# Optimization experiments

Hardware: AMD Instinct MI355X
Metric: run time of the kernel (lower is better)

Reference implementation:

```python
import jax, jax.numpy as jnp
import numpy as np
from jax import lax

BATCH = 2560
N_CLS = 128    # QP decision dim n
N_INEQ = 128   # number of inequality constraints
N_FEAT = 128
IPM_ITERS = 20
SIGMA = 0.1    # centering parameter


def setup_inputs() -> dict:
    key = jax.random.key(0)
    k1, k2, k3, k4, k5 = jax.random.split(key, 5)
    x = jax.random.normal(k1, (BATCH, N_FEAT), dtype=jnp.float32)
    # symmetric positive-definite Q (qpth requires PD Q)
    A = jax.random.normal(k2, (N_CLS, N_CLS), dtype=jnp.float32) / np.sqrt(N_CLS).astype(np.float32)
    Q = A @ A.T + 1e-4 * jnp.eye(N_CLS, dtype=jnp.float32)
    p = jax.random.normal(k3, (BATCH, N_CLS), dtype=jnp.float32)
    G = jax.random.uniform(k4, (N_INEQ, N_CLS), minval=-1.0, maxval=1.0, dtype=jnp.float32)
    # h > 0 so z = 0 is strictly feasible -> well-conditioned IPM
    h = jax.random.uniform(k5, (N_INEQ,), dtype=jnp.float32) + 1.0
    return {"x": x, "Q": Q, "p": p, "G": G, "h": h, "m": 1}


def _qp_solve(Q, p, G, h, iters=IPM_ITERS, sigma=SIGMA):
    """Batched primal-dual interior-point solve of
       min_z 1/2 z'Qz + p'z  s.t.  Gz + s = h, s >= 0.
    Q: [n,n] shared; p: [B,n]; G: [m,n] shared; h: [m] shared."""
    B, n = p.shape
    mI = G.shape[0]
    z = jnp.zeros((B, n), p.dtype)
    s = jnp.ones((B, mI), p.dtype)
    lam = jnp.ones((B, mI), p.dtype)
    GT = G.T

    def frac_to_boundary(v, dv):
        safe = jnp.where(dv < 0, dv, -1.0)
        r = jnp.where(dv < 0, -v / safe, 1e9)
        return jnp.minimum(1.0, 0.99 * jnp.min(r, axis=1, keepdims=True))

    def step(carry, _):
        z, s, lam = carry
        r_d = z @ Q.T + p + lam @ G          # [B,n]  Qz + p + G'lam
        r_p = z @ GT + s - h                 # [B,m]  Gz + s - h
        mu = jnp.mean(s * lam, axis=1, keepdims=True)
        r_c = s * lam - sigma * mu           # [B,m]
        d = lam / s                          # [B,m]
        # reduced KKT: (Q + G' D G) dz = -r_d + G'((r_c - lam*r_p)/s)
        M = Q[None] + jnp.einsum('ki,bk,kj->bij', G, d, G)  # [B,n,n]
        rhs = -r_d + ((r_c - lam * r_p) / s) @ G             # [B,n]
        dz = jnp.linalg.solve(M, rhs[..., None])[..., 0]
        ds = -r_p - dz @ GT
        dlam = (-r_c - lam * ds) / s
        a = jnp.minimum(frac_to_boundary(s, ds), frac_to_boundary(lam, dlam))
        return (z + a * dz, s + a * ds, lam + a * dlam), None

    (z, s, lam), _ = lax.scan(step, (z, s, lam), None, length=iters)
    return z


def reference(x, Q, p, G, h, m):
    # m==1 path of OptNet.forward: p stays [B,n], Q shared [n,n]
    pf = p.T if m > 1 else p
    z = _qp_solve(Q.astype(jnp.float32), pf.astype(jnp.float32),
                  G.astype(jnp.float32), h.astype(jnp.float32))
    out = z.reshape(10, -1)  # faithful to x.view(10, -1)
    return jax.nn.log_softmax(out, axis=1)
```

## Files before the change

### kernel.cpp

```cpp
#include <hip/hip_runtime.h>
#include <math.h>


#define B_TOT 2560
#define TB 32
#define NB (B_TOT/TB)

__device__ __forceinline__ int ROFF(int i){ return (i*(i+1))>>1; }
__device__ __forceinline__ int rowStart(int i){
  int a=i>>2, b=i&3;
  return ((a+1)*((a<<1)+b))<<2;
}
#define TRI_SZ 8448

__device__ __forceinline__ int rowOfIdx(int idx){
  int i = (int)((sqrtf(8.f*(float)idx+1.f)-1.f)*0.5f);
  while (((i+1)*(i+2)>>1) <= idx) ++i;
  while (((i*(i+1))>>1) > idx) --i;
  return i;
}

__device__ __forceinline__ void chol_diag_gj(float* tri, int c0, int lane){
  float rowA[16], rowW[16];
  const int r = lane;
  #pragma unroll
  for (int j=0;j<16;++j){ rowA[j]=0.f; rowW[j]=0.f; }
  if (r < 16){
    const float* src = &tri[rowStart(c0+r)+c0];
    #pragma unroll
    for (int q=0;q<4;++q){
      if (q <= (r>>2)){
        float4 w = *(const float4*)&src[4*q];
        rowA[4*q+0]=w.x; rowA[4*q+1]=w.y; rowA[4*q+2]=w.z; rowA[4*q+3]=w.w;
      }
    }
    #pragma unroll
    for (int j=0;j<16;++j) if (j>r) rowA[j]=0.f;
    #pragma unroll
    for (int j=0;j<16;++j) rowW[j] = (j==r)?1.f:0.f;
  }
  #pragma unroll
  for (int k=0;k<16;++k){
    float akk = __shfl(rowA[k], k, 64);
    akk = fmaxf(akk, 1e-12f);
    float linv = rsqrtf(akk);
    float lrk = rowA[k]*linv;
    if (r==k){
      #pragma unroll
      for (int c=0;c<16;++c) rowW[c] *= linv;
    }
    #pragma unroll
    for (int j=k+1;j<16;++j){
      float ljk = __shfl(lrk, j, 64);
      if (r>=j) rowA[j] = fmaf(-lrk, ljk, rowA[j]);
    }
    #pragma unroll
    for (int c=0;c<=k;++c){
      float wkc = __shfl(rowW[c], k, 64);
      if (r>k) rowW[c] = fmaf(-lrk, wkc, rowW[c]);
    }
  }
  if (r < 16){
    float* dst = &tri[rowStart(c0+r)+c0];
    #pragma unroll
    for (int q=0;q<4;++q){
      if (q <= (r>>2)){
        float4 w; w.x=rowW[4*q+0]; w.y=rowW[4*q+1]; w.z=rowW[4*q+2]; w.w=rowW[4*q+3];
        *(float4*)&dst[4*q] = w;
      }
    }
  }
}

__device__ void chol_factor(float* tri, int t, int lane, int wid){
  for (int kb=0; kb<8; ++kb){
    const int c0 = kb*16;
    if (wid==(kb&3)) chol_diag_gj(tri, c0, lane);
    __syncthreads();
    const int rem = 112 - c0;
    if (t < rem){
      const int r = c0+16+t;
      const int rb = rowStart(r)+c0;
      float a[16];
      #pragma unroll
      for (int q=0;q<4;++q){
        float4 w = *(const float4*)&tri[rb+4*q];
        a[4*q+0]=w.x; a[4*q+1]=w.y; a[4*q+2]=w.z; a[4*q+3]=w.w;
      }
      float x[16];
      #pragma unroll
      for (int c=0;c<16;++c){
        float acc=0.f;
        const int lb = rowStart(c0+c)+c0;
        #pragma unroll
        for (int q=0;q<=(c>>2);++q){
          float4 w = *(const float4*)&tri[lb+4*q];
          if (4*q+0<=c) acc = fmaf(w.x, a[4*q+0], acc);
          if (4*q+1<=c) acc = fmaf(w.y, a[4*q+1], acc);
          if (4*q+2<=c) acc = fmaf(w.z, a[4*q+2], acc);
          if (4*q+3<=c) acc = fmaf(w.w, a[4*q+3], acc);
        }
        x[c]=acc;
      }
      #pragma unroll
      for (int q=0;q<4;++q){
        float4 w; w.x=x[4*q+0]; w.y=x[4*q+1]; w.z=x[4*q+2]; w.w=x[4*q+3];
        *(float4*)&tri[rb+4*q] = w;
      }
    }
    __syncthreads();
    if (rem > 0){
      const int base = c0+16;
      const int R = rem>>2;
      const int ntile = (R*(R+1))>>1;
      for (int idx=t; idx<ntile; idx+=256){
        int I = rowOfIdx(idx);
        int J = idx - ROFF(I);
        int i0 = base + 4*I, j0 = base + 4*J;
        int ra0=rowStart(i0+0)+c0, ra1=rowStart(i0+1)+c0,
            ra2=rowStart(i0+2)+c0, ra3=rowStart(i0+3)+c0;
        int rb0=rowStart(j0+0)+c0, rb1=rowStart(j0+1)+c0,
            rb2=rowStart(j0+2)+c0, rb3=rowStart(j0+3)+c0;
        float acc[4][4];
        #pragma unroll
        for (int ii=0;ii<4;++ii)
          #pragma unroll
          for (int jj=0;jj<4;++jj) acc[ii][jj]=0.f;
        #pragma unroll
        for (int q=0;q<4;++q){
          float4 A0=*(const float4*)&tri[ra0+4*q];
          float4 A1=*(const float4*)&tri[ra1+4*q];
          float4 A2=*(const float4*)&tri[ra2+4*q];
          float4 A3=*(const float4*)&tri[ra3+4*q];
          float4 B0=*(const float4*)&tri[rb0+4*q];
          float4 B1=*(const float4*)&tri[rb1+4*q];
          float4 B2=*(const float4*)&tri[rb2+4*q];
          float4 B3=*(const float4*)&tri[rb3+4*q];
          #define DOT4(Ai,Bj) (fmaf(Ai.x,Bj.x,fmaf(Ai.y,Bj.y,fmaf(Ai.z,Bj.z,Ai.w*Bj.w))))
          acc[0][0]+=DOT4(A0,B0); acc[0][1]+=DOT4(A0,B1); acc[0][2]+=DOT4(A0,B2); acc[0][3]+=DOT4(A0,B3);
          acc[1][0]+=DOT4(A1,B0); acc[1][1]+=DOT4(A1,B1); acc[1][2]+=DOT4(A1,B2); acc[1][3]+=DOT4(A1,B3);
          acc[2][0]+=DOT4(A2,B0); acc[2][1]+=DOT4(A2,B1); acc[2][2]+=DOT4(A2,B2); acc[2][3]+=DOT4(A2,B3);
          acc[3][0]+=DOT4(A3,B0); acc[3][1]+=DOT4(A3,B1); acc[3][2]+=DOT4(A3,B2); acc[3][3]+=DOT4(A3,B3);
          #undef DOT4
        }
        #pragma unroll
        for (int ii=0;ii<4;++ii){
          #pragma unroll
          for (int jj=0;jj<4;++jj){
            int gi=i0+ii, gj=j0+jj;
            if (gi>=gj) tri[rowStart(gi)+gj] -= acc[ii][jj];
          }
        }
      }
    }
    __syncthreads();
  }
}

__device__ void chol_factor_w2(float* tri, int t, int lane, int wid){
  for (int kb=0; kb<8; ++kb){
    const int c0 = kb*16;
    if (wid==0) chol_diag_gj(tri, c0, lane);
    __syncthreads();
    const int rem = 112 - c0;
    if (t < rem){
      const int r = c0+16+t;
      const int rb = rowStart(r)+c0;
      float a[16];
      #pragma unroll
      for (int q=0;q<4;++q){
        float4 w = *(const float4*)&tri[rb+4*q];
        a[4*q+0]=w.x; a[4*q+1]=w.y; a[4*q+2]=w.z; a[4*q+3]=w.w;
      }
      float x[16];
      #pragma unroll
      for (int c=0;c<16;++c){
        float acc=0.f;
        const int lb = rowStart(c0+c)+c0;
        #pragma unroll
        for (int q=0;q<=(c>>2);++q){
          float4 w = *(const float4*)&tri[lb+4*q];
          if (4*q+0<=c) acc = fmaf(w.x, a[4*q+0], acc);
          if (4*q+1<=c) acc = fmaf(w.y, a[4*q+1], acc);
          if (4*q+2<=c) acc = fmaf(w.z, a[4*q+2], acc);
          if (4*q+3<=c) acc = fmaf(w.w, a[4*q+3], acc);
        }
        x[c]=acc;
      }
      #pragma unroll
      for (int q=0;q<4;++q){
        float4 w; w.x=x[4*q+0]; w.y=x[4*q+1]; w.z=x[4*q+2]; w.w=x[4*q+3];
        *(float4*)&tri[rb+4*q] = w;
      }
    }
    __syncthreads();
    if (rem > 0){
      const int base = c0+16;
      const int R = rem>>2;
      const int ntile = (R*(R+1))>>1;
      for (int idx=t; idx<ntile; idx+=128){
        int I = rowOfIdx(idx);
        int J = idx - ROFF(I);
        int i0 = base + 4*I, j0 = base + 4*J;
        int ra0=rowStart(i0+0)+c0, ra1=rowStart(i0+1)+c0,
            ra2=rowStart(i0+2)+c0, ra3=rowStart(i0+3)+c0;
        int rb0=rowStart(j0+0)+c0, rb1=rowStart(j0+1)+c0,
            rb2=rowStart(j0+2)+c0, rb3=rowStart(j0+3)+c0;
        float acc[4][4];
        #pragma unroll
        for (int ii=0;ii<4;++ii)
          #pragma unroll
          for (int jj=0;jj<4;++jj) acc[ii][jj]=0.f;
        #pragma unroll
        for (int q=0;q<4;++q){
          float4 A0=*(const float4*)&tri[ra0+4*q];
          float4 A1=*(const float4*)&tri[ra1+4*q];
          float4 A2=*(const float4*)&tri[ra2+4*q];
          float4 A3=*(const float4*)&tri[ra3+4*q];
          float4 B0=*(const float4*)&tri[rb0+4*q];
          float4 B1=*(const float4*)&tri[rb1+4*q];
          float4 B2=*(const float4*)&tri[rb2+4*q];
          float4 B3=*(const float4*)&tri[rb3+4*q];
          #define DOT4(Ai,Bj) (fmaf(Ai.x,Bj.x,fmaf(Ai.y,Bj.y,fmaf(Ai.z,Bj.z,Ai.w*Bj.w))))
          acc[0][0]+=DOT4(A0,B0); acc[0][1]+=DOT4(A0,B1); acc[0][2]+=DOT4(A0,B2); acc[0][3]+=DOT4(A0,B3);
          acc[1][0]+=DOT4(A1,B0); acc[1][1]+=DOT4(A1,B1); acc[1][2]+=DOT4(A1,B2); acc[1][3]+=DOT4(A1,B3);
          acc[2][0]+=DOT4(A2,B0); acc[2][1]+=DOT4(A2,B1); acc[2][2]+=DOT4(A2,B2); acc[2][3]+=DOT4(A2,B3);
          acc[3][0]+=DOT4(A3,B0); acc[3][1]+=DOT4(A3,B1); acc[3][2]+=DOT4(A3,B2); acc[3][3]+=DOT4(A3,B3);
          #undef DOT4
        }
        #pragma unroll
        for (int ii=0;ii<4;++ii){
          #pragma unroll
          for (int jj=0;jj<4;++jj){
            int gi=i0+ii, gj=j0+jj;
            if (gi>=gj) tri[rowStart(gi)+gj] -= acc[ii][jj];
          }
        }
      }
    }
    __syncthreads();
  }
}

__device__ void tri_solve_w2(const float* tri, float* rhs, int t){
  for (int kb=0;kb<8;++kb){
    const int c0=kb*16;
    if (t<16){
      const int c=t;
      const float* lrow = &tri[rowStart(c0+c)+c0];
      float acc=0.f;
      #pragma unroll
      for (int cp=0;cp<16;++cp) if (cp<=c) acc = fmaf(lrow[cp], rhs[c0+cp], acc);
      rhs[c0+c] = acc;
    }
    __syncthreads();
    const int rem = 112-c0;
    if (t<rem){
      const int r = c0+16+t;
      const int rb = rowStart(r)+c0;
      float acc = rhs[r];
      #pragma unroll
      for (int q=0;q<4;++q){
        float4 w = *(const float4*)&tri[rb+4*q];
        acc = fmaf(-w.x, rhs[c0+4*q+0], acc);
        acc = fmaf(-w.y, rhs[c0+4*q+1], acc);
        acc = fmaf(-w.z, rhs[c0+4*q+2], acc);
        acc = fmaf(-w.w, rhs[c0+4*q+3], acc);
      }
      rhs[r] = acc;
    }
    __syncthreads();
  }
  for (int kb=7;kb>=0;--kb){
    const int c0=kb*16;
    if (t<16){
      const int c=t;
      float acc=0.f;
      #pragma unroll
      for (int cp=0;cp<16;++cp)
        if (cp>=c) acc = fmaf(tri[rowStart(c0+cp)+c0+c], rhs[c0+cp], acc);
      rhs[c0+c] = acc;
    }
    __syncthreads();
    if (t<c0){
      float acc = rhs[t];
      #pragma unroll
      for (int c=0;c<16;++c) acc = fmaf(-tri[rowStart(c0+c)+t], rhs[c0+c], acc);
      rhs[t]=acc;
    }
    __syncthreads();
  }
}

__global__ __launch_bounds__(256) void k_prep(const float* __restrict__ Q,
        const float* __restrict__ Gm, float* __restrict__ Qi, float* __restrict__ M1)
{
  __shared__ __align__(16) float tri[TRI_SZ];
  __shared__ float Xl[128*32];
  const int t = threadIdx.x;
  const int lane = t&63, wid = t>>6;
  for (int idx=t; idx<8256; idx+=256){
    int i = rowOfIdx(idx); int j = idx - ROFF(i);
    tri[rowStart(i)+j] = Q[i*128+j];
  }
  __syncthreads();
  chol_factor(tri, t, lane, wid);
  for (int cc=0; cc<8; ++cc){
    const int a0 = (cc&3)*32;
    const bool ident = (cc<4);
    for (int idx=t; idx<4096; idx+=256){
      int i=idx>>5, j=idx&31;
      Xl[idx] = ident ? ((i==(a0+j))?1.f:0.f) : Gm[(a0+j)*128+i];
    }
    __syncthreads();
    for (int kb=0;kb<8;++kb){
      const int c0=kb*16;
      if (t<32){
        float v[16], x[16];
        #pragma unroll
        for (int c=0;c<16;++c) v[c]=Xl[(c0+c)*32+t];
        #pragma unroll
        for (int c=0;c<16;++c){
          float acc=0.f;
          const int lb=rowStart(c0+c)+c0;
          #pragma unroll
          for (int cp=0;cp<16;++cp) if (cp<=c) acc=fmaf(tri[lb+cp], v[cp], acc);
          x[c]=acc;
        }
        #pragma unroll
        for (int c=0;c<16;++c) Xl[(c0+c)*32+t]=x[c];
      }
      __syncthreads();
      const int rem=112-c0;
      for (int rr=(t>>5); rr<rem; rr+=8){
        const int r=c0+16+rr, j=t&31;
        float acc=Xl[r*32+j];
        #pragma unroll
        for (int c=0;c<16;++c) acc = fmaf(-tri[rowStart(r)+c0+c], Xl[(c0+c)*32+j], acc);
        Xl[r*32+j]=acc;
      }
      __syncthreads();
    }
    for (int kb=7;kb>=0;--kb){
      const int c0=kb*16;
      if (t<32){
        float v[16], x[16];
        #pragma unroll
        for (int c=0;c<16;++c) v[c]=Xl[(c0+c)*32+t];
        #pragma unroll
        for (int c=0;c<16;++c){
          float acc=0.f;
          #pragma unroll
          for (int cp=0;cp<16;++cp) if (cp>=c) acc=fmaf(tri[rowStart(c0+cp)+c0+c], v[cp], acc);
          x[c]=acc;
        }
        #pragma unroll
        for (int c=0;c<16;++c) Xl[(c0+c)*32+t]=x[c];
      }
      __syncthreads();
      for (int rr=(t>>5); rr<c0; rr+=8){
        const int j=t&31;
        float acc=Xl[rr*32+j];
        #pragma unroll
        for (int c=0;c<16;++c) acc = fmaf(-tri[rowStart(c0+c)+rr], Xl[(c0+c)*32+j], acc);
        Xl[rr*32+j]=acc;
      }
      __syncthreads();
    }
    float* dst = ident ? Qi : M1;
    for (int idx=t; idx<4096; idx+=256){
      int i=idx>>5, j=idx&31;
      dst[i*128+a0+j] = Xl[idx];
    }
    __syncthreads();
  }
}

__global__ __launch_bounds__(256) void k_kmat(const float* __restrict__ Gm,
        const float* __restrict__ M1, float* __restrict__ K, float* __restrict__ Kd){
  const int idx = blockIdx.x*256 + threadIdx.x;
  const int a = idx>>7, bcol = idx&127;
  float a0=0.f,a1=0.f,a2=0.f,a3=0.f;
  #pragma unroll
  for (int j=0;j<128;j+=4){
    a0 = fmaf(Gm[a*128+j+0], M1[(j+0)*128+bcol], a0);
    a1 = fmaf(Gm[a*128+j+1], M1[(j+1)*128+bcol], a1);
    a2 = fmaf(Gm[a*128+j+2], M1[(j+2)*128+bcol], a2);
    a3 = fmaf(Gm[a*128+j+3], M1[(j+3)*128+bcol], a3);
  }
  float acc = (a0+a1)+(a2+a3);
  K[idx] = acc;
  if (a==bcol) Kd[a]=acc;
}

__global__ __launch_bounds__(256) void k_init(const float* __restrict__ p,
    float* __restrict__ Pt, float* __restrict__ S, float* __restrict__ LAM,
    float* __restrict__ GZ, float* __restrict__ QZ, float* __restrict__ Zst){
  int idx = blockIdx.x*256 + threadIdx.x;
  if (idx < 128*B_TOT){
    int i = idx/B_TOT, b = idx - i*B_TOT;
    Pt[idx] = p[b*128+i];
    S[idx]=1.f; LAM[idx]=1.f; GZ[idx]=0.f; QZ[idx]=0.f; Zst[idx]=0.f;
  }
}

__global__ __launch_bounds__(256) void k_B(const float* __restrict__ G,
    const float* __restrict__ M1, const float* __restrict__ Pt,
    const float* __restrict__ h,
    const float* __restrict__ S, const float* __restrict__ LAM,
    const float* __restrict__ GZ, const float* __restrict__ QZ,
    float* __restrict__ RHS, float* __restrict__ TV){
  __shared__ float wm_l[128*33];
  __shared__ float rhs_l[128*33];
  __shared__ float part_l[8*33];
  __shared__ float mu_l[TB];
  __shared__ float h_l[128];
  const int t=threadIdx.x, g=t>>5, bl=t&31;
  const int b = blockIdx.x*TB + bl;
  if (t<128) h_l[t]=h[t];
  __syncthreads();
  float sv[16], lv[16], rpv[16];
  float prod=0.f;
  #pragma unroll
  for (int q=0;q<16;++q){
    int i = g + 8*q;
    float s = S[i*B_TOT+b], l = LAM[i*B_TOT+b], gz = GZ[i*B_TOT+b];
    sv[q]=s; lv[q]=l; rpv[q]=gz+s-h_l[i];
    prod += s*l;
  }
  part_l[g*33+bl] = prod;
  __syncthreads();
  if (g==0){
    float m=0.f;
    #pragma unroll
    for (int q=0;q<8;++q) m += part_l[q*33+bl];
    mu_l[bl] = m*(1.f/128.f);
  }
  __syncthreads();
  const float mu = mu_l[bl];
  #pragma unroll
  for (int q=0;q<16;++q){
    int i=g+8*q;
    float rc = sv[q]*lv[q] - 0.1f*mu;
    wm_l[i*33+bl] = (rc - lv[q]*rpv[q])/sv[q] - lv[q];
  }
  __syncthreads();
  const int r0 = g*16;
  float acc[16];
  #pragma unroll
  for (int q=0;q<16;++q) acc[q] = -(QZ[(r0+q)*B_TOT+b] + Pt[(r0+q)*B_TOT+b]);
  #pragma unroll 2
  for (int j=0;j<128;++j){
    float wmv = wm_l[j*33+bl];
    const float4* gp = (const float4*)&G[j*128+r0];
    #pragma unroll
    for (int q4=0;q4<4;++q4){
      float4 gv = gp[q4];
      acc[4*q4+0]=fmaf(gv.x,wmv,acc[4*q4+0]);
      acc[4*q4+1]=fmaf(gv.y,wmv,acc[4*q4+1]);
      acc[4*q4+2]=fmaf(gv.z,wmv,acc[4*q4+2]);
      acc[4*q4+3]=fmaf(gv.w,wmv,acc[4*q4+3]);
    }
  }
  #pragma unroll
  for (int q=0;q<16;++q){
    rhs_l[(r0+q)*33+bl]=acc[q];
    RHS[(r0+q)*B_TOT+b]=acc[q];
  }
  __syncthreads();
  #pragma unroll
  for (int q=0;q<16;++q) acc[q]=0.f;
  #pragma unroll 2
  for (int j=0;j<128;++j){
    float rv = rhs_l[j*33+bl];
    const float4* mp = (const float4*)&M1[j*128+r0];
    #pragma unroll
    for (int q4=0;q4<4;++q4){
      float4 mv = mp[q4];
      acc[4*q4+0]=fmaf(mv.x,rv,acc[4*q4+0]);
      acc[4*q4+1]=fmaf(mv.y,rv,acc[4*q4+1]);
      acc[4*q4+2]=fmaf(mv.z,rv,acc[4*q4+2]);
      acc[4*q4+3]=fmaf(mv.w,rv,acc[4*q4+3]);
    }
  }
  #pragma unroll
  for (int q=0;q<16;++q) TV[(r0+q)*B_TOT+b]=acc[q];
}

__global__ __launch_bounds__(128) void k_C(const float* __restrict__ K,
    const float* __restrict__ Kd, const float* __restrict__ h,
    const float* __restrict__ TV,
    float* __restrict__ S, float* __restrict__ LAM, float* __restrict__ GZ,
    float* __restrict__ Y, float* __restrict__ ALPHA){
  __shared__ __align__(16) float tri[TRI_SZ];
  __shared__ float scl_l[128];
  __shared__ float sh_t[128];
  __shared__ float red[2];
  const int t = threadIdx.x, b = blockIdx.x;
  const int lane = t&63, wid = t>>6;
  float s_t=S[t*B_TOT+b], l_t=LAM[t*B_TOT+b], g_t=GZ[t*B_TOT+b];
  float rp_t = g_t + s_t - h[t];
  float prod = s_t*l_t;
  #pragma unroll
  for (int o=32;o>0;o>>=1) prod += __shfl_xor(prod,o,64);
  if (lane==0) red[wid]=prod;
  __syncthreads();
  const float mu = (red[0]+red[1])*(1.f/128.f);
  float rc_t = s_t*l_t - 0.1f*mu;
  float di_t = fminf(s_t/l_t, 1e30f);
  float sc_t = rsqrtf(Kd[t]+di_t);
  scl_l[t]=sc_t;
  sh_t[t]=TV[t*B_TOT+b]*sc_t;
  __syncthreads();
  #pragma unroll 4
  for (int i=0;i<128;++i){
    if (t<=i){
      tri[rowStart(i)+t] = (t==i)?1.f : K[i*128+t]*scl_l[i]*sc_t;
    }
  }
  __syncthreads();
  chol_factor_w2(tri, t, lane, wid);
  tri_solve_w2(tri, sh_t, t);
  float y = sh_t[t]*sc_t;
  float gd = di_t*y;
  float ds = -rp_t - gd;
  float dl = (-rc_t - l_t*ds)/s_t;
  float ra = 1e9f;
  if (ds<0.f) ra = -s_t/ds;
  if (dl<0.f) ra = fminf(ra,-l_t/dl);
  #pragma unroll
  for (int o=32;o>0;o>>=1) ra = fminf(ra,__shfl_xor(ra,o,64));
  __syncthreads();
  if (lane==0) red[wid]=ra;
  __syncthreads();
  const float alpha = fminf(1.0f, 0.99f*fminf(red[0],red[1]));
  S[t*B_TOT+b]   = s_t + alpha*ds;
  LAM[t*B_TOT+b] = l_t + alpha*dl;
  GZ[t*B_TOT+b]  = g_t + alpha*gd;
  Y[t*B_TOT+b]   = y;
  if (t==0) ALPHA[b]=alpha;
}

__global__ __launch_bounds__(256) void k_D(const float* __restrict__ G,
    const float* __restrict__ Qi, const float* __restrict__ RHS,
    const float* __restrict__ Y, const float* __restrict__ ALPHA,
    float* __restrict__ Zst, float* __restrict__ QZ){
  __shared__ float y_l[128*33];
  __shared__ float v_l[128*33];
  const int t=threadIdx.x, g=t>>5, bl=t&31;
  const int b = blockIdx.x*TB + bl;
  #pragma unroll
  for (int q=0;q<16;++q){
    int i=g+8*q;
    y_l[i*33+bl] = Y[i*B_TOT+b];
  }
  const float alpha = ALPHA[b];
  __syncthreads();
  const int r0=g*16;
  float acc[16];
  #pragma unroll
  for (int q=0;q<16;++q) acc[q]=RHS[(r0+q)*B_TOT+b];
  #pragma unroll 2
  for (int j=0;j<128;++j){
    float yv = y_l[j*33+bl];
    const float4* gp=(const float4*)&G[j*128+r0];
    #pragma unroll
    for (int q4=0;q4<4;++q4){
      float4 gv=gp[q4];
      acc[4*q4+0]=fmaf(-gv.x,yv,acc[4*q4+0]);
      acc[4*q4+1]=fmaf(-gv.y,yv,acc[4*q4+1]);
      acc[4*q4+2]=fmaf(-gv.z,yv,acc[4*q4+2]);
      acc[4*q4+3]=fmaf(-gv.w,yv,acc[4*q4+3]);
    }
  }
  #pragma unroll
  for (int q=0;q<16;++q){
    v_l[(r0+q)*33+bl]=acc[q];
    float* qp=&QZ[(r0+q)*B_TOT+b];
    *qp = *qp + alpha*acc[q];
  }
  __syncthreads();
  #pragma unroll
  for (int q=0;q<16;++q) acc[q]=0.f;
  #pragma unroll 2
  for (int j=0;j<128;++j){
    float vv = v_l[j*33+bl];
    const float4* qp4=(const float4*)&Qi[j*128+r0];
    #pragma unroll
    for (int q4=0;q4<4;++q4){
      float4 qv=qp4[q4];
      acc[4*q4+0]=fmaf(qv.x,vv,acc[4*q4+0]);
      acc[4*q4+1]=fmaf(qv.y,vv,acc[4*q4+1]);
      acc[4*q4+2]=fmaf(qv.z,vv,acc[4*q4+2]);
      acc[4*q4+3]=fmaf(qv.w,vv,acc[4*q4+3]);
    }
  }
  #pragma unroll
  for (int q=0;q<16;++q){
    float* zp=&Zst[(r0+q)*B_TOT+b];
    *zp = *zp + alpha*acc[q];
  }
}

__global__ __launch_bounds__(1024) void k_logsoftmax(const float* __restrict__ Zst,
                                                     float* __restrict__ out){
  __shared__ float red[16];
  __shared__ float sval[2];
  const int r = blockIdx.x, t = threadIdx.x;
  float m = -1e30f;
  for (int k=t;k<32768;k+=1024){
    float v = Zst[(k&127)*B_TOT + r*256 + (k>>7)];
    m = fmaxf(m, v);
  }
  #pragma unroll
  for (int o=32;o>0;o>>=1) m = fmaxf(m, __shfl_down(m,o,64));
  if ((t&63)==0) red[t>>6] = m;
  __syncthreads();
  if (t==0){ float mm=red[0]; for (int w=1;w<16;++w) mm=fmaxf(mm,red[w]); sval[0]=mm; }
  __syncthreads();
  const float mx = sval[0];
  float s=0.f;
  for (int k=t;k<32768;k+=1024){
    float v = Zst[(k&127)*B_TOT + r*256 + (k>>7)];
    s += expf(v-mx);
  }
  #pragma unroll
  for (int o=32;o>0;o>>=1) s += __shfl_down(s,o,64);
  if ((t&63)==0) red[t>>6]=s;
  __syncthreads();
  if (t==0){ float ss=0.f; for (int w=0;w<16;++w) ss+=red[w]; sval[1]=logf(ss); }
  __syncthreads();
  const float lse = sval[1];
  for (int k=t;k<32768;k+=1024){
    float v = Zst[(k&127)*B_TOT + r*256 + (k>>7)];
    out[(size_t)r*32768+k] = v-mx-lse;
  }
}

extern "C" void kernel_launch(void* const* d_in, const int* in_sizes, int n_in,
                              void* d_out, int out_size, void* d_ws, size_t ws_size,
                              hipStream_t stream){
  const float* Q = (const float*)d_in[1];
  const float* p = (const float*)d_in[2];
  const float* G = (const float*)d_in[3];
  const float* h = (const float*)d_in[4];
  float* ws  = (float*)d_ws;
  const int NE = 128*B_TOT;
  float* Zst = ws;
  float* Qi  = Zst + NE;
  float* M1  = Qi + 16384;
  float* K   = M1 + 16384;
  float* Kd  = K + 16384;
  float* ALPHA = Kd + 128;
  float* Pt  = ALPHA + 2560;
  float* S   = Pt + NE;
  float* LAM = S + NE;
  float* GZ  = LAM + NE;
  float* QZ  = GZ + NE;
  float* RHS = QZ + NE;
  float* TV  = RHS + NE;
  float* Y   = TV + NE;
  float* out = (float*)d_out;

  hipLaunchKernelGGL(k_prep, dim3(1), dim3(256), 0, stream, Q, G, Qi, M1);
  hipLaunchKernelGGL(k_kmat, dim3(64), dim3(256), 0, stream, G, M1, K, Kd);
  hipLaunchKernelGGL(k_init, dim3((NE+255)/256), dim3(256), 0, stream,
                     p, Pt, S, LAM, GZ, QZ, Zst);
  for (int it=0; it<20; ++it){
    hipLaunchKernelGGL(k_B, dim3(NB), dim3(256), 0, stream,
                       G, M1, Pt, h, S, LAM, GZ, QZ, RHS, TV);
    hipLaunchKernelGGL(k_C, dim3(B_TOT), dim3(128), 0, stream,
                       K, Kd, h, TV, S, LAM, GZ, Y, ALPHA);
    hipLaunchKernelGGL(k_D, dim3(NB), dim3(256), 0, stream,
                       G, Qi, RHS, Y, ALPHA, Zst, QZ);
  }
  hipLaunchKernelGGL(k_logsoftmax, dim3(10), dim3(1024), 0, stream, Zst, out);
}
```

Measured before the change: 8.739 ms.

## Batch Cholesky across 16 problems per block with global batch-interleaved factor storage

Measured after the change: 14.28 ms. 63.4% more time.

```diff
diff --git a/kernel.cpp b/kernel.cpp
--- a/kernel.cpp
+++ b/kernel.cpp
@@ -5,6 +5,8 @@
 #define B_TOT 2560
 #define TB 32
 #define NB (B_TOT/TB)
+#define BT 16
+#define NBC (B_TOT/BT)
 
 __device__ __forceinline__ int ROFF(int i){ return (i*(i+1))>>1; }
 __device__ __forceinline__ int rowStart(int i){
@@ -157,141 +159,6 @@
   }
 }
 
-__device__ void chol_factor_w2(float* tri, int t, int lane, int wid){
-  for (int kb=0; kb<8; ++kb){
-    const int c0 = kb*16;
-    if (wid==0) chol_diag_gj(tri, c0, lane);
-    __syncthreads();
-    const int rem = 112 - c0;
-    if (t < rem){
-      const int r = c0+16+t;
-      const int rb = rowStart(r)+c0;
-      float a[16];
-      #pragma unroll
-      for (int q=0;q<4;++q){
-        float4 w = *(const float4*)&tri[rb+4*q];
-        a[4*q+0]=w.x; a[4*q+1]=w.y; a[4*q+2]=w.z; a[4*q+3]=w.w;
-      }
-      float x[16];
-      #pragma unroll
-      for (int c=0;c<16;++c){
-        float acc=0.f;
-        const int lb = rowStart(c0+c)+c0;
-        #pragma unroll
-        for (int q=0;q<=(c>>2);++q){
-          float4 w = *(const float4*)&tri[lb+4*q];
-          if (4*q+0<=c) acc = fmaf(w.x, a[4*q+0], acc);
-          if (4*q+1<=c) acc = fmaf(w.y, a[4*q+1], acc);
-          if (4*q+2<=c) acc = fmaf(w.z, a[4*q+2], acc);
-          if (4*q+3<=c) acc = fmaf(w.w, a[4*q+3], acc);
-        }
-        x[c]=acc;
-      }
-      #pragma unroll
-      for (int q=0;q<4;++q){
-        float4 w; w.x=x[4*q+0]; w.y=x[4*q+1]; w.z=x[4*q+2]; w.w=x[4*q+3];
-        *(float4*)&tri[rb+4*q] = w;
-      }
-    }
-    __syncthreads();
-    if (rem > 0){
-      const int base = c0+16;
-      const int R = rem>>2;
-      const int ntile = (R*(R+1))>>1;
-      for (int idx=t; idx<ntile; idx+=128){
-        int I = rowOfIdx(idx);
-        int J = idx - ROFF(I);
-        int i0 = base + 4*I, j0 = base + 4*J;
-        int ra0=rowStart(i0+0)+c0, ra1=rowStart(i0+1)+c0,
-            ra2=rowStart(i0+2)+c0, ra3=rowStart(i0+3)+c0;
-        int rb0=rowStart(j0+0)+c0, rb1=rowStart(j0+1)+c0,
-            rb2=rowStart(j0+2)+c0, rb3=rowStart(j0+3)+c0;
-        float acc[4][4];
-        #pragma unroll
-        for (int ii=0;ii<4;++ii)
-          #pragma unroll
-          for (int jj=0;jj<4;++jj) acc[ii][jj]=0.f;
-        #pragma unroll
-        for (int q=0;q<4;++q){
-          float4 A0=*(const float4*)&tri[ra0+4*q];
-          float4 A1=*(const float4*)&tri[ra1+4*q];
-          float4 A2=*(const float4*)&tri[ra2+4*q];
-          float4 A3=*(const float4*)&tri[ra3+4*q];
-          float4 B0=*(const float4*)&tri[rb0+4*q];
-          float4 B1=*(const float4*)&tri[rb1+4*q];
-          float4 B2=*(const float4*)&tri[rb2+4*q];
-          float4 B3=*(const float4*)&tri[rb3+4*q];
-          #define DOT4(Ai,Bj) (fmaf(Ai.x,Bj.x,fmaf(Ai.y,Bj.y,fmaf(Ai.z,Bj.z,Ai.w*Bj.w))))
-          acc[0][0]+=DOT4(A0,B0); acc[0][1]+=DOT4(A0,B1); acc[0][2]+=DOT4(A0,B2); acc[0][3]+=DOT4(A0,B3);
-          acc[1][0]+=DOT4(A1,B0); acc[1][1]+=DOT4(A1,B1); acc[1][2]+=DOT4(A1,B2); acc[1][3]+=DOT4(A1,B3);
-          acc[2][0]+=DOT4(A2,B0); acc[2][1]+=DOT4(A2,B1); acc[2][2]+=DOT4(A2,B2); acc[2][3]+=DOT4(A2,B3);
-          acc[3][0]+=DOT4(A3,B0); acc[3][1]+=DOT4(A3,B1); acc[3][2]+=DOT4(A3,B2); acc[3][3]+=DOT4(A3,B3);
-          #undef DOT4
-        }
-        #pragma unroll
-        for (int ii=0;ii<4;++ii){
-          #pragma unroll
-          for (int jj=0;jj<4;++jj){
-            int gi=i0+ii, gj=j0+jj;
-            if (gi>=gj) tri[rowStart(gi)+gj] -= acc[ii][jj];
-          }
-        }
-      }
-    }
-    __syncthreads();
-  }
-}
-
-__device__ void tri_solve_w2(const float* tri, float* rhs, int t){
-  for (int kb=0;kb<8;++kb){
-    const int c0=kb*16;
-    if (t<16){
-      const int c=t;
-      const float* lrow = &tri[rowStart(c0+c)+c0];
-      float acc=0.f;
-      #pragma unroll
-      for (int cp=0;cp<16;++cp) if (cp<=c) acc = fmaf(lrow[cp], rhs[c0+cp], acc);
-      rhs[c0+c] = acc;
-    }
-    __syncthreads();
-    const int rem = 112-c0;
-    if (t<rem){
-      const int r = c0+16+t;
-      const int rb = rowStart(r)+c0;
-      float acc = rhs[r];
-      #pragma unroll
-      for (int q=0;q<4;++q){
-        float4 w = *(const float4*)&tri[rb+4*q];
-        acc = fmaf(-w.x, rhs[c0+4*q+0], acc);
-        acc = fmaf(-w.y, rhs[c0+4*q+1], acc);
-        acc = fmaf(-w.z, rhs[c0+4*q+2], acc);
-        acc = fmaf(-w.w, rhs[c0+4*q+3], acc);
-      }
-      rhs[r] = acc;
-    }
-    __syncthreads();
-  }
-  for (int kb=7;kb>=0;--kb){
-    const int c0=kb*16;
-    if (t<16){
-      const int c=t;
-      float acc=0.f;
-      #pragma unroll
-      for (int cp=0;cp<16;++cp)
-        if (cp>=c) acc = fmaf(tri[rowStart(c0+cp)+c0+c], rhs[c0+cp], acc);
-      rhs[c0+c] = acc;
-    }
-    __syncthreads();
-    if (t<c0){
-      float acc = rhs[t];
-      #pragma unroll
-      for (int c=0;c<16;++c) acc = fmaf(-tri[rowStart(c0+c)+t], rhs[c0+c], acc);
-      rhs[t]=acc;
-    }
-    __syncthreads();
-  }
-}
-
 __global__ __launch_bounds__(256) void k_prep(const float* __restrict__ Q,
         const float* __restrict__ Gm, float* __restrict__ Qi, float* __restrict__ M1)
 {
@@ -487,58 +354,276 @@
   for (int q=0;q<16;++q) TV[(r0+q)*B_TOT+b]=acc[q];
 }
 
-__global__ __launch_bounds__(128) void k_C(const float* __restrict__ K,
-    const float* __restrict__ Kd, const float* __restrict__ h,
-    const float* __restrict__ TV,
+__global__ __launch_bounds__(512) void k_Cfac(
+    const float* __restrict__ K, const float* __restrict__ Kd,
+    const float* __restrict__ h, const float* __restrict__ TV,
     float* __restrict__ S, float* __restrict__ LAM, float* __restrict__ GZ,
-    float* __restrict__ Y, float* __restrict__ ALPHA){
-  __shared__ __align__(16) float tri[TRI_SZ];
-  __shared__ float scl_l[128];
-  __shared__ float sh_t[128];
-  __shared__ float red[2];
-  const int t = threadIdx.x, b = blockIdx.x;
-  const int lane = t&63, wid = t>>6;
-  float s_t=S[t*B_TOT+b], l_t=LAM[t*B_TOT+b], g_t=GZ[t*B_TOT+b];
-  float rp_t = g_t + s_t - h[t];
-  float prod = s_t*l_t;
-  #pragma unroll
-  for (int o=32;o>0;o>>=1) prod += __shfl_xor(prod,o,64);
-  if (lane==0) red[wid]=prod;
-  __syncthreads();
-  const float mu = (red[0]+red[1])*(1.f/128.f);
-  float rc_t = s_t*l_t - 0.1f*mu;
-  float di_t = fminf(s_t/l_t, 1e30f);
-  float sc_t = rsqrtf(Kd[t]+di_t);
-  scl_l[t]=sc_t;
-  sh_t[t]=TV[t*B_TOT+b]*sc_t;
-  __syncthreads();
-  #pragma unroll 4
+    float* __restrict__ TRI, float* __restrict__ Y, float* __restrict__ ALPHA)
+{
+  __shared__ float scl[128*16];
+  __shared__ float rhs[128*16];
+  __shared__ float Dg[136*17];
+  __shared__ float part[32*17];
+  __shared__ float muv[16], alp[16];
+  __shared__ unsigned char r16[136];
+  const int t = threadIdx.x;
+  const int bl = t & 15, rw = t >> 4;
+  const int lane = t & 63, wid = t >> 6;
+  const int b0 = blockIdx.x * BT;
+  const int b = b0 + bl;
+
+  if (t < 136) r16[t] = (unsigned char)rowOfIdx(t);
+
+  float prod = 0.f;
+  #pragma unroll
+  for (int q=0;q<4;++q){
+    int i = rw + 32*q;
+    prod = fmaf(S[i*B_TOT+b], LAM[i*B_TOT+b], prod);
+  }
+  part[rw*17+bl] = prod;
+  __syncthreads();
+  if (t < 16){
+    float m=0.f;
+    #pragma unroll
+    for (int r=0;r<32;++r) m += part[r*17+t];
+    muv[t] = m*(1.f/128.f);
+  }
+  __syncthreads();
+  #pragma unroll
+  for (int q=0;q<4;++q){
+    int i = rw + 32*q;
+    float s = S[i*B_TOT+b], l = LAM[i*B_TOT+b];
+    float di = fminf(s/l, 1e30f);
+    float sc = rsqrtf(Kd[i]+di);
+    scl[i*16+bl] = sc;
+    rhs[i*16+bl] = TV[i*B_TOT+b]*sc;
+  }
+  __syncthreads();
+
   for (int i=0;i<128;++i){
-    if (t<=i){
-      tri[rowStart(i)+t] = (t==i)?1.f : K[i*128+t]*scl_l[i]*sc_t;
-    }
-  }
-  __syncthreads();
-  chol_factor_w2(tri, t, lane, wid);
-  tri_solve_w2(tri, sh_t, t);
-  float y = sh_t[t]*sc_t;
-  float gd = di_t*y;
-  float ds = -rp_t - gd;
-  float dl = (-rc_t - l_t*ds)/s_t;
+    const int base = ROFF(i);
+    const float sci = scl[i*16+bl];
+    for (int j=rw; j<=i; j+=32){
+      float v = (j==i)? 1.f : K[i*128+j]*sci*scl[j*16+bl];
+      TRI[(base+j)*B_TOT + b] = v;
+    }
+  }
+  __syncthreads();
+
+  for (int kb=0;kb<8;++kb){
+    const int c0 = 16*kb;
+    const int rem = 112 - c0;
+    for (int u=t; u<2176; u+=512){
+      int idx = u>>4, bt = u&15;
+      int r = r16[idx], c = idx - ((r*(r+1))>>1);
+      Dg[idx*17+bt] = TRI[(ROFF(c0+r)+c0+c)*B_TOT + b0+bt];
+    }
+    __syncthreads();
+    if (wid < 4){
+      const int r = lane & 15, bat = wid*4 + (lane>>4);
+      float rowA[16], rowW[16];
+      #pragma unroll
+      for (int j=0;j<16;++j){
+        rowA[j] = (j<=r)? Dg[(((r*(r+1))>>1)+j)*17 + bat] : 0.f;
+        rowW[j] = (j==r)? 1.f : 0.f;
+      }
+      #pragma unroll
+      for (int k=0;k<16;++k){
+        float akk = __shfl(rowA[k], (lane&48)|k, 64);
+        akk = fmaxf(akk, 1e-12f);
+        float linv = rsqrtf(akk);
+        float lrk = rowA[k]*linv;
+        if (r==k){
+          #pragma unroll
+          for (int c=0;c<16;++c) rowW[c] *= linv;
+        }
+        #pragma unroll
+        for (int j=k+1;j<16;++j){
+          float ljk = __shfl(lrk, (lane&48)|j, 64);
+          if (r>=j) rowA[j] = fmaf(-lrk, ljk, rowA[j]);
+        }
+        #pragma unroll
+        for (int c=0;c<=k;++c){
+          float wkc = __shfl(rowW[c], (lane&48)|k, 64);
+          if (r>k) rowW[c] = fmaf(-lrk, wkc, rowW[c]);
+        }
+      }
+      #pragma unroll
+      for (int c=0;c<16;++c)
+        if (c<=r) Dg[(((r*(r+1))>>1)+c)*17 + bat] = rowW[c];
+    }
+    __syncthreads();
+    for (int u=t; u<2176; u+=512){
+      int idx = u>>4, bt = u&15;
+      int r = r16[idx], c = idx - ((r*(r+1))>>1);
+      TRI[(ROFF(c0+r)+c0+c)*B_TOT + b0+bt] = Dg[idx*17+bt];
+    }
+    for (int rr=rw; rr<rem; rr+=32){
+      const int r = c0+16+rr;
+      const int rb = ROFF(r)+c0;
+      float a[16], x[16];
+      #pragma unroll
+      for (int c=0;c<16;++c) a[c] = TRI[(rb+c)*B_TOT + b];
+      #pragma unroll
+      for (int c=0;c<16;++c){
+        float acc=0.f;
+        const int lb = ((c*(c+1))>>1)*17;
+        #pragma unroll
+        for (int cp=0;cp<16;++cp)
+          if (cp<=c) acc = fmaf(Dg[lb + cp*17 + bl], a[cp], acc);
+        x[c]=acc;
+      }
+      #pragma unroll
+      for (int c=0;c<16;++c) TRI[(rb+c)*B_TOT + b] = x[c];
+    }
+    __syncthreads();
+    if (rem > 0){
+      const int base = c0+16;
+      const int nBk = rem>>4;
+      const int nunits = ((nBk*(nBk+1))>>1)*4;
+      for (int u=rw; u<nunits; u+=32){
+        const int pidx = u>>2, sub = u&3;
+        int bI = rowOfIdx(pidx);
+        int bJ = pidx - ((bI*(bI+1))>>1);
+        const int si = sub>>1, sj = sub&1;
+        if (bI==bJ && sj>si) continue;
+        const int i0 = base + 16*bI + 8*si;
+        const int j0 = base + 16*bJ + 8*sj;
+        int eI[8], eJ[8];
+        #pragma unroll
+        for (int ii=0;ii<8;++ii) eI[ii] = (ROFF(i0+ii)+c0)*B_TOT + b;
+        #pragma unroll
+        for (int jj=0;jj<8;++jj) eJ[jj] = (ROFF(j0+jj)+c0)*B_TOT + b;
+        float acc[8][8];
+        #pragma unroll
+        for (int ii=0;ii<8;++ii)
+          #pragma unroll
+          for (int jj=0;jj<8;++jj) acc[ii][jj]=0.f;
+        #pragma unroll 4
+        for (int k=0;k<16;++k){
+          float LI[8], LJ[8];
+          #pragma unroll
+          for (int ii=0;ii<8;++ii) LI[ii] = TRI[eI[ii] + k*B_TOT];
+          #pragma unroll
+          for (int jj=0;jj<8;++jj) LJ[jj] = TRI[eJ[jj] + k*B_TOT];
+          #pragma unroll
+          for (int ii=0;ii<8;++ii)
+            #pragma unroll
+            for (int jj=0;jj<8;++jj)
+              acc[ii][jj] = fmaf(LI[ii], LJ[jj], acc[ii][jj]);
+        }
+        const bool dsub = (bI==bJ && si==sj);
+        #pragma unroll
+        for (int ii=0;ii<8;++ii){
+          const int rb2 = ROFF(i0+ii);
+          #pragma unroll
+          for (int jj=0;jj<8;++jj){
+            if (dsub && jj>ii) continue;
+            const int e = (rb2 + j0+jj)*B_TOT + b;
+            TRI[e] -= acc[ii][jj];
+          }
+        }
+      }
+    }
+    __syncthreads();
+  }
+
+  for (int kb=0;kb<8;++kb){
+    const int c0=16*kb, rem=112-c0;
+    for (int u=t; u<2176; u+=512){
+      int idx=u>>4, bt=u&15;
+      int r=r16[idx], c=idx-((r*(r+1))>>1);
+      Dg[idx*17+bt] = TRI[(ROFF(c0+r)+c0+c)*B_TOT + b0+bt];
+    }
+    __syncthreads();
+    float accd=0.f;
+    if (t<256){
+      const int c=t>>4, blx=t&15;
+      #pragma unroll
+      for (int cp=0;cp<16;++cp)
+        if (cp<=c) accd = fmaf(Dg[(((c*(c+1))>>1)+cp)*17+blx],
+                               rhs[(c0+cp)*16+blx], accd);
+    }
+    __syncthreads();
+    if (t<256) rhs[(c0+(t>>4))*16+(t&15)] = accd;
+    __syncthreads();
+    for (int rr=rw; rr<rem; rr+=32){
+      const int r=c0+16+rr;
+      const int rb=ROFF(r)+c0;
+      float a2 = rhs[r*16+bl];
+      #pragma unroll
+      for (int c=0;c<16;++c)
+        a2 = fmaf(-TRI[(rb+c)*B_TOT+b], rhs[(c0+c)*16+bl], a2);
+      rhs[r*16+bl] = a2;
+    }
+    __syncthreads();
+  }
+  for (int kb=7;kb>=0;--kb){
+    const int c0=16*kb;
+    for (int u=t; u<2176; u+=512){
+      int idx=u>>4, bt=u&15;
+      int r=r16[idx], c=idx-((r*(r+1))>>1);
+      Dg[idx*17+bt] = TRI[(ROFF(c0+r)+c0+c)*B_TOT + b0+bt];
+    }
+    __syncthreads();
+    float accd=0.f;
+    if (t<256){
+      const int c=t>>4, blx=t&15;
+      #pragma unroll
+      for (int cp=0;cp<16;++cp)
+        if (cp>=c) accd = fmaf(Dg[(((cp*(cp+1))>>1)+c)*17+blx],
+                               rhs[(c0+cp)*16+blx], accd);
+    }
+    __syncthreads();
+    if (t<256) rhs[(c0+(t>>4))*16+(t&15)] = accd;
+    __syncthreads();
+    for (int r=rw; r<c0; r+=32){
+      float a2 = rhs[r*16+bl];
+      #pragma unroll
+      for (int c=0;c<16;++c)
+        a2 = fmaf(-TRI[(ROFF(c0+c)+r)*B_TOT+b], rhs[(c0+c)*16+bl], a2);
+      rhs[r*16+bl] = a2;
+    }
+    __syncthreads();
+  }
+
+  float s4[4],l4[4],g4[4],ds4[4],dl4[4],gd4[4],y4[4];
   float ra = 1e9f;
-  if (ds<0.f) ra = -s_t/ds;
-  if (dl<0.f) ra = fminf(ra,-l_t/dl);
-  #pragma unroll
-  for (int o=32;o>0;o>>=1) ra = fminf(ra,__shfl_xor(ra,o,64));
-  __syncthreads();
-  if (lane==0) red[wid]=ra;
-  __syncthreads();
-  const float alpha = fminf(1.0f, 0.99f*fminf(red[0],red[1]));
-  S[t*B_TOT+b]   = s_t + alpha*ds;
-  LAM[t*B_TOT+b] = l_t + alpha*dl;
-  GZ[t*B_TOT+b]  = g_t + alpha*gd;
-  Y[t*B_TOT+b]   = y;
-  if (t==0) ALPHA[b]=alpha;
+  const float mu = muv[bl];
+  #pragma unroll
+  for (int q=0;q<4;++q){
+    int i = rw+32*q;
+    float s=S[i*B_TOT+b], l=LAM[i*B_TOT+b], g=GZ[i*B_TOT+b];
+    float rp = g+s-h[i];
+    float rc = s*l - 0.1f*mu;
+    float di = fminf(s/l,1e30f);
+    float y = rhs[i*16+bl]*scl[i*16+bl];
+    float gd = di*y;
+    float ds = -rp-gd;
+    float dl = (-rc-l*ds)/s;
+    if (ds<0.f) ra = fminf(ra,-s/ds);
+    if (dl<0.f) ra = fminf(ra,-l/dl);
+    s4[q]=s;l4[q]=l;g4[q]=g;ds4[q]=ds;dl4[q]=dl;gd4[q]=gd;y4[q]=y;
+  }
+  part[rw*17+bl]=ra;
+  __syncthreads();
+  if (t<16){
+    float m=1e9f;
+    #pragma unroll
+    for (int r=0;r<32;++r) m=fminf(m,part[r*17+t]);
+    alp[t]=fminf(1.0f, 0.99f*m);
+  }
+  __syncthreads();
+  const float alpha = alp[bl];
+  #pragma unroll
+  for (int q=0;q<4;++q){
+    int i=rw+32*q;
+    S[i*B_TOT+b]  = s4[q]+alpha*ds4[q];
+    LAM[i*B_TOT+b]= l4[q]+alpha*dl4[q];
+    GZ[i*B_TOT+b] = g4[q]+alpha*gd4[q];
+    Y[i*B_TOT+b]  = y4[q];
+  }
+  if (t<16) ALPHA[b0+t]=alp[t];
 }
 
 __global__ __launch_bounds__(256) void k_D(const float* __restrict__ G,
@@ -660,6 +745,7 @@
   float* RHS = QZ + NE;
   float* TV  = RHS + NE;
   float* Y   = TV + NE;
+  float* TRI = Y + NE;
   float* out = (float*)d_out;
 
   hipLaunchKernelGGL(k_prep, dim3(1), dim3(256), 0, stream, Q, G, Qi, M1);
@@ -669,8 +755,8 @@
   for (int it=0; it<20; ++it){
     hipLaunchKernelGGL(k_B, dim3(NB), dim3(256), 0, stream,
                        G, M1, Pt, h, S, LAM, GZ, QZ, RHS, TV);
-    hipLaunchKernelGGL(k_C, dim3(B_TOT), dim3(128), 0, stream,
-                       K, Kd, h, TV, S, LAM, GZ, Y, ALPHA);
+    hipLaunchKernelGGL(k_Cfac, dim3(NBC), dim3(512), 0, stream,
+                       K, Kd, h, TV, S, LAM, GZ, TRI, Y, ALPHA);
     hipLaunchKernelGGL(k_D, dim3(NB), dim3(256), 0, stream,
                        G, Qi, RHS, Y, ALPHA, Zst, QZ);
   }
```
